# Kernel optimization log

Measured on AMD Instinct MI355X. Metric: run time of the kernel, lower is better.

## Reference

```python
import jax, jax.numpy as jnp
import numpy as np

N = 100000      # number of edge features (rows of feats)
M = 800000      # number of triplets
HID = 128
HEADS = 8
DH = HID // HEADS


def setup_inputs() -> dict:
    key = jax.random.key(0)
    ks = jax.random.split(key, 10)
    s = 1.0 / np.sqrt(HID)
    inp = {
        "feats": jax.random.normal(ks[0], (N, HID), dtype=jnp.float32),
        "idx_kj": jax.random.randint(ks[1], (M,), 0, N, dtype=jnp.int64),
        "idx_ji": jax.random.randint(ks[2], (M,), 0, N, dtype=jnp.int64),
        "Wv": jax.random.uniform(ks[3], (HID, HID), jnp.float32, -s, s),
        "Wq": jax.random.uniform(ks[4], (HID, HID), jnp.float32, -s, s),
        "Wk": jax.random.uniform(ks[5], (HID, HID), jnp.float32, -s, s),
        "W1": jax.random.uniform(ks[6], (HID, HID), jnp.float32, -s, s),
        "b1": jax.random.uniform(ks[7], (HID,), jnp.float32, -s, s),
        "W2": jax.random.uniform(ks[8], (HID, HID), jnp.float32, -s, s),
        "b2": jax.random.uniform(ks[9], (HID,), jnp.float32, -s, s),
    }
    return inp


def reference(feats, idx_kj, idx_ji, Wv, Wq, Wk, W1, b1, W2, b2):
    # Projections (no bias), reshape to [N, H, Dh]
    v = (feats @ Wv.T).reshape(N, HEADS, DH)
    k = (feats @ Wk.T).reshape(N, HEADS, DH)
    q = (feats @ Wq.T).reshape(N, HEADS, DH)

    # edge-indexed attention scores: [M, H, 1]
    att = jnp.sum(q[idx_kj] * k[idx_ji], axis=-1, keepdims=True)
    att = jnp.exp(jax.nn.leaky_relu(att, negative_slope=0.2))  # unsafe softmax, as in source

    # segment-sum normalizer over destination index idx_ji: [N, H, 1]
    denom = jax.ops.segment_sum(att, idx_ji, num_segments=N)
    att = att / denom[idx_ji]

    # weighted V gather-scatter: [M, HID] -> [N, HID]
    v_att = (v[idx_kj] * att).reshape(M, HID)
    agg = jax.ops.segment_sum(v_att, idx_ji, num_segments=N)  # v_clone after +scatter-v

    v_flat = v.reshape(N, HID)
    # ResidualLayer (dropout in eval mode -> identity): v + relu(lin2(relu(lin1(agg))))
    h = jax.nn.relu(agg @ W1.T + b1)
    h = jax.nn.relu(h @ W2.T + b2)
    return v_flat + h
```

## Files before the change

### kernel.cpp

```cpp
#include <hip/hip_runtime.h>
#include <hip/hip_bf16.h>
#include <math.h>

#define N_NODES 100000
#define M_EDGES 800000
#define HID 128
#define HEADS 8
#define DH 16
#define SCAN_NB ((N_NODES + 1023) / 1024)

typedef __attribute__((ext_vector_type(8))) short short8;
typedef __attribute__((ext_vector_type(4))) float floatx4;

__device__ __forceinline__ ushort f32_to_bf16(float x) {
    __hip_bfloat16 h = __float2bfloat16(x);
    union { __hip_bfloat16 h; ushort u; } c; c.h = h;
    return c.u;
}
__device__ __forceinline__ float bf16_bits_to_f32(ushort u) {
    union { unsigned int i; float f; } c; c.i = ((unsigned int)u) << 16;
    return c.f;
}
__device__ __forceinline__ float bf16pair_lo(unsigned int p) {
    union { unsigned int i; float f; } c; c.i = p << 16; return c.f;
}
__device__ __forceinline__ float bf16pair_hi(unsigned int p) {
    union { unsigned int i; float f; } c; c.i = p & 0xffff0000u; return c.f;
}

__device__ __forceinline__ void stage_w_frag(const ushort* __restrict__ W,
                                             ushort* __restrict__ lds, int tid)
{
    #pragma unroll
    for (int i = 0; i < 8; ++i) {
        int idx  = i * 256 + tid;
        int f    = idx >> 6;
        int lane = idx & 63;
        int t    = f & 7, ks = f >> 3;
        int row  = t * 16 + (lane & 15);
        int col  = ks * 32 + (lane >> 4) * 8;
        uint4 d = *(const uint4*)(W + row * HID + col);
        *(uint4*)(lds + idx * 8) = d;
    }
}

__global__ __launch_bounds__(256) void cvt_w_kernel(
    const float* __restrict__ Wq, const float* __restrict__ Wk, const float* __restrict__ Wv,
    const float* __restrict__ W1, const float* __restrict__ W2,
    ushort* __restrict__ dq, ushort* __restrict__ dk, ushort* __restrict__ dv,
    ushort* __restrict__ d1, ushort* __restrict__ d2)
{
    int i = blockIdx.x * 256 + threadIdx.x;
    int w = i >> 14;
    int j = i & 16383;
    const float* s[5] = {Wq, Wk, Wv, W1, W2};
    ushort*      d[5] = {dq, dk, dv, d1, d2};
    d[w][j] = f32_to_bf16(s[w][j]);
}

__global__ __launch_bounds__(256) void qkv_mfma_kernel(
    const float* __restrict__ feats,
    const ushort* __restrict__ Wq16, const ushort* __restrict__ Wk16, const ushort* __restrict__ Wv16,
    ushort* __restrict__ qv16, ushort* __restrict__ k16)
{
    __shared__ ushort wlds[16384];
    const int tid  = threadIdx.x;
    const int wave = tid >> 6;
    const int lane = tid & 63;
    const int row0 = blockIdx.x * 128 + wave * 32;
    const int lrow = lane & 15;
    const int lk   = (lane >> 4) * 8;
    const int crow = (lane >> 4) * 4;

    short8 afrag[2][4];
    bool tvalid[2];
    #pragma unroll
    for (int r = 0; r < 2; ++r) {
        int rr = row0 + r * 16;
        tvalid[r] = (rr < N_NODES);
        const float* arow = feats + (size_t)((tvalid[r] ? rr : 0) + lrow) * HID + lk;
        #pragma unroll
        for (int ks = 0; ks < 4; ++ks) {
            float4 f0 = *(const float4*)(arow + ks * 32);
            float4 f1 = *(const float4*)(arow + ks * 32 + 4);
            short8 a;
            a[0] = (short)f32_to_bf16(f0.x); a[1] = (short)f32_to_bf16(f0.y);
            a[2] = (short)f32_to_bf16(f0.z); a[3] = (short)f32_to_bf16(f0.w);
            a[4] = (short)f32_to_bf16(f1.x); a[5] = (short)f32_to_bf16(f1.y);
            a[6] = (short)f32_to_bf16(f1.z); a[7] = (short)f32_to_bf16(f1.w);
            afrag[r][ks] = a;
        }
    }

    const ushort* Ws[3] = {Wq16, Wk16, Wv16};
    ushort* Ob[3]; int Ostride[3];
    Ob[0] = qv16;       Ostride[0] = 256;
    Ob[1] = k16;        Ostride[1] = 128;
    Ob[2] = qv16 + 128; Ostride[2] = 256;

    #pragma unroll
    for (int w = 0; w < 3; ++w) {
        __syncthreads();
        stage_w_frag(Ws[w], wlds, tid);
        __syncthreads();

        floatx4 acc[2][8];
        #pragma unroll
        for (int r = 0; r < 2; ++r)
            #pragma unroll
            for (int t = 0; t < 8; ++t) acc[r][t] = (floatx4)(0.f);

        #pragma unroll
        for (int ks = 0; ks < 4; ++ks) {
            short8 B[8];
            #pragma unroll
            for (int t = 0; t < 8; ++t)
                B[t] = *(const short8*)&wlds[(ks * 8 + t) * 512 + lane * 8];
            #pragma unroll
            for (int t = 0; t < 8; ++t) {
                acc[0][t] = __builtin_amdgcn_mfma_f32_16x16x32_bf16(B[t], afrag[0][ks], acc[0][t], 0, 0, 0);
                acc[1][t] = __builtin_amdgcn_mfma_f32_16x16x32_bf16(B[t], afrag[1][ks], acc[1][t], 0, 0, 0);
            }
        }

        #pragma unroll
        for (int r = 0; r < 2; ++r) {
            if (tvalid[r]) {
                ushort* O = Ob[w] + (size_t)(row0 + r * 16 + lrow) * Ostride[w];
                #pragma unroll
                for (int t = 0; t < 8; ++t) {
                    ushort4 o;
                    o.x = f32_to_bf16(acc[r][t][0]); o.y = f32_to_bf16(acc[r][t][1]);
                    o.z = f32_to_bf16(acc[r][t][2]); o.w = f32_to_bf16(acc[r][t][3]);
                    *(ushort4*)(O + t * 16 + crow) = o;
                }
            }
        }
    }
}

__global__ __launch_bounds__(256) void hist_kernel(
    const int* __restrict__ idx_ji, int* __restrict__ count)
{
    int m = blockIdx.x * 256 + threadIdx.x;
    if (m < M_EDGES) atomicAdd(&count[idx_ji[m]], 1);
}

__global__ __launch_bounds__(256) void scan_blocksum_kernel(
    const int* __restrict__ count, int* __restrict__ blocksum)
{
    __shared__ int s[256];
    const int tid = threadIdx.x;
    const int base = blockIdx.x * 1024 + tid * 4;
    int sum = 0;
    if (base + 3 < N_NODES) {
        int4 c = *(const int4*)(count + base);
        sum = c.x + c.y + c.z + c.w;
    } else {
        #pragma unroll
        for (int j = 0; j < 4; ++j) if (base + j < N_NODES) sum += count[base + j];
    }
    s[tid] = sum;
    __syncthreads();
    for (int off = 128; off > 0; off >>= 1) {
        if (tid < off) s[tid] += s[tid + off];
        __syncthreads();
    }
    if (tid == 0) blocksum[blockIdx.x] = s[0];
}

__global__ __launch_bounds__(128) void scan_top_kernel(int* __restrict__ blocksum)
{
    __shared__ int s[128];
    const int t = threadIdx.x;
    int v = (t < SCAN_NB) ? blocksum[t] : 0;
    s[t] = v;
    __syncthreads();
    for (int off = 1; off < 128; off <<= 1) {
        int x = (t >= off) ? s[t - off] : 0;
        __syncthreads();
        s[t] += x;
        __syncthreads();
    }
    if (t < SCAN_NB) blocksum[t] = s[t] - v;
}

__global__ __launch_bounds__(256) void scan_write_kernel(
    const int* __restrict__ count, const int* __restrict__ blocksum,
    int* __restrict__ offsets, int* __restrict__ cursor)
{
    __shared__ int s[256];
    const int tid = threadIdx.x;
    const int base = blockIdx.x * 1024 + tid * 4;
    int c0 = 0, c1 = 0, c2 = 0, c3 = 0;
    if (base + 3 < N_NODES) {
        int4 c = *(const int4*)(count + base);
        c0 = c.x; c1 = c.y; c2 = c.z; c3 = c.w;
    } else {
        if (base     < N_NODES) c0 = count[base];
        if (base + 1 < N_NODES) c1 = count[base + 1];
        if (base + 2 < N_NODES) c2 = count[base + 2];
        if (base + 3 < N_NODES) c3 = count[base + 3];
    }
    const int tsum = c0 + c1 + c2 + c3;
    s[tid] = tsum;
    __syncthreads();
    for (int off = 1; off < 256; off <<= 1) {
        int x = (tid >= off) ? s[tid - off] : 0;
        __syncthreads();
        s[tid] += x;
        __syncthreads();
    }
    int o0 = s[tid] - tsum + blocksum[blockIdx.x];
    int o1 = o0 + c0, o2 = o1 + c1, o3 = o2 + c2;
    if (base + 3 < N_NODES) {
        *(int4*)(offsets + base) = make_int4(o0, o1, o2, o3);
        *(int4*)(cursor  + base) = make_int4(o0, o1, o2, o3);
    } else {
        if (base     < N_NODES) { offsets[base]     = o0; cursor[base]     = o0; }
        if (base + 1 < N_NODES) { offsets[base + 1] = o1; cursor[base + 1] = o1; }
        if (base + 2 < N_NODES) { offsets[base + 2] = o2; cursor[base + 2] = o2; }
        if (base + 3 < N_NODES) { offsets[base + 3] = o3; cursor[base + 3] = o3; }
    }
}

__global__ __launch_bounds__(256) void fill_kernel(
    const int* __restrict__ idx_ji, const int* __restrict__ idx_kj,
    int* __restrict__ cursor, int* __restrict__ edge_kj)
{
    int m = blockIdx.x * 256 + threadIdx.x;
    if (m < M_EDGES) {
        int pos = atomicAdd(&cursor[idx_ji[m]], 1);
        edge_kj[pos] = idx_kj[m];
    }
}

__global__ __launch_bounds__(256) void aggregate_kernel(
    const int* __restrict__ edge_kj, const int* __restrict__ offsets,
    const int* __restrict__ count, const ushort* __restrict__ qv16,
    const ushort* __restrict__ k16, ushort* __restrict__ agg16)
{
    const int gid  = blockIdx.x * 256 + threadIdx.x;
    const int node = gid >> 4;
    const int l16  = threadIdx.x & 15;
    if (node >= N_NODES) return;

    const int deg  = count[node];
    const int base = offsets[node];

    float kn[8];
    {
        uint4 kp = *(const uint4*)(k16 + (size_t)node * HID + l16 * 8);
        const unsigned int* kw = (const unsigned int*)&kp;
        #pragma unroll
        for (int j = 0; j < 4; ++j) {
            kn[2*j]   = bf16pair_lo(kw[j]);
            kn[2*j+1] = bf16pair_hi(kw[j]);
        }
    }

    float acc[8] = {0.f,0.f,0.f,0.f,0.f,0.f,0.f,0.f};
    float d = 0.f;

    int e = 0;
    for (; e + 2 <= deg; e += 2) {
        const int kj0 = edge_kj[base + e];
        const int kj1 = edge_kj[base + e + 1];
        const ushort* r0 = qv16 + (size_t)kj0 * 256 + l16 * 8;
        const ushort* r1 = qv16 + (size_t)kj1 * 256 + l16 * 8;
        uint4 qp0 = *(const uint4*)r0;
        uint4 vp0 = *(const uint4*)(r0 + 128);
        uint4 qp1 = *(const uint4*)r1;
        uint4 vp1 = *(const uint4*)(r1 + 128);

        const unsigned int* q0 = (const unsigned int*)&qp0;
        const unsigned int* q1 = (const unsigned int*)&qp1;
        float p0 = 0.f, p1 = 0.f;
        #pragma unroll
        for (int j = 0; j < 4; ++j) {
            p0 += bf16pair_lo(q0[j]) * kn[2*j] + bf16pair_hi(q0[j]) * kn[2*j+1];
            p1 += bf16pair_lo(q1[j]) * kn[2*j] + bf16pair_hi(q1[j]) * kn[2*j+1];
        }
        p0 += __shfl_xor(p0, 1);
        p1 += __shfl_xor(p1, 1);
        float lr0 = (p0 >= 0.f) ? p0 : 0.2f * p0;
        float lr1 = (p1 >= 0.f) ? p1 : 0.2f * p1;
        float s0 = __expf(lr0);
        float s1 = __expf(lr1);
        d += s0 + s1;
        const unsigned int* v0 = (const unsigned int*)&vp0;
        const unsigned int* v1 = (const unsigned int*)&vp1;
        #pragma unroll
        for (int j = 0; j < 4; ++j) {
            acc[2*j]   += s0 * bf16pair_lo(v0[j]) + s1 * bf16pair_lo(v1[j]);
            acc[2*j+1] += s0 * bf16pair_hi(v0[j]) + s1 * bf16pair_hi(v1[j]);
        }
    }
    if (e < deg) {
        const int kj0 = edge_kj[base + e];
        const ushort* r0 = qv16 + (size_t)kj0 * 256 + l16 * 8;
        uint4 qp0 = *(const uint4*)r0;
        uint4 vp0 = *(const uint4*)(r0 + 128);
        const unsigned int* q0 = (const unsigned int*)&qp0;
        float p0 = 0.f;
        #pragma unroll
        for (int j = 0; j < 4; ++j)
            p0 += bf16pair_lo(q0[j]) * kn[2*j] + bf16pair_hi(q0[j]) * kn[2*j+1];
        p0 += __shfl_xor(p0, 1);
        float lr0 = (p0 >= 0.f) ? p0 : 0.2f * p0;
        float s0 = __expf(lr0);
        d += s0;
        const unsigned int* v0 = (const unsigned int*)&vp0;
        #pragma unroll
        for (int j = 0; j < 4; ++j) {
            acc[2*j]   += s0 * bf16pair_lo(v0[j]);
            acc[2*j+1] += s0 * bf16pair_hi(v0[j]);
        }
    }

    const float inv = (deg > 0) ? 1.f / d : 0.f;
    uint4 o;
    unsigned int* ow = (unsigned int*)&o;
    #pragma unroll
    for (int j = 0; j < 4; ++j)
        ow[j] = (unsigned int)f32_to_bf16(acc[2*j] * inv)
              | ((unsigned int)f32_to_bf16(acc[2*j+1] * inv) << 16);
    *(uint4*)(agg16 + (size_t)node * HID + l16 * 8) = o;
}

__global__ __launch_bounds__(256) void mlp_mfma_kernel(
    const ushort* __restrict__ agg16, const ushort* __restrict__ qv16,
    const ushort* __restrict__ W1_16, const float* __restrict__ b1,
    const ushort* __restrict__ W2_16, const float* __restrict__ b2,
    float* __restrict__ out)
{
    __shared__ ushort wlds[16384];
    __shared__ ushort h1s[16384];
    const int tid  = threadIdx.x;
    const int wave = tid >> 6;
    const int lane = tid & 63;
    const int row0 = blockIdx.x * 128 + wave * 32;
    const int lrow = lane & 15;
    const int lk   = (lane >> 4) * 8;
    const int crow = (lane >> 4) * 4;

    short8 afrag[2][4];
    bool tvalid[2];
    #pragma unroll
    for (int r = 0; r < 2; ++r) {
        int rr = row0 + r * 16;
        tvalid[r] = (rr < N_NODES);
        const ushort* arow = agg16 + (size_t)((tvalid[r] ? rr : 0) + lrow) * HID + lk;
        #pragma unroll
        for (int ks = 0; ks < 4; ++ks)
            afrag[r][ks] = *(const short8*)(arow + ks * 32);
    }

    stage_w_frag(W1_16, wlds, tid);
    __syncthreads();

    {
        floatx4 acc[2][8];
        #pragma unroll
        for (int r = 0; r < 2; ++r)
            #pragma unroll
            for (int t = 0; t < 8; ++t) acc[r][t] = (floatx4)(0.f);
        #pragma unroll
        for (int ks = 0; ks < 4; ++ks) {
            short8 B[8];
            #pragma unroll
            for (int t = 0; t < 8; ++t)
                B[t] = *(const short8*)&wlds[(ks * 8 + t) * 512 + lane * 8];
            #pragma unroll
            for (int t = 0; t < 8; ++t) {
                acc[0][t] = __builtin_amdgcn_mfma_f32_16x16x32_bf16(B[t], afrag[0][ks], acc[0][t], 0, 0, 0);
                acc[1][t] = __builtin_amdgcn_mfma_f32_16x16x32_bf16(B[t], afrag[1][ks], acc[1][t], 0, 0, 0);
            }
        }
        #pragma unroll
        for (int r = 0; r < 2; ++r) {
            ushort* tile = &h1s[(wave * 2 + r) * 2048];
            #pragma unroll
            for (int t = 0; t < 8; ++t) {
                float4 bias = *(const float4*)(b1 + t * 16 + crow);
                ushort4 o;
                o.x = f32_to_bf16(fmaxf(acc[r][t][0] + bias.x, 0.f));
                o.y = f32_to_bf16(fmaxf(acc[r][t][1] + bias.y, 0.f));
                o.z = f32_to_bf16(fmaxf(acc[r][t][2] + bias.z, 0.f));
                o.w = f32_to_bf16(fmaxf(acc[r][t][3] + bias.w, 0.f));
                int ks   = t >> 1;
                int quad = (t & 1) * 2 + (crow >> 3);
                int j0   = crow & 4;
                *(ushort4*)(tile + (ks * 64 + quad * 16 + lrow) * 8 + j0) = o;
            }
        }
    }
    __syncthreads();
    stage_w_frag(W2_16, wlds, tid);
    __syncthreads();

    {
        short8 hfrag[2][4];
        #pragma unroll
        for (int r = 0; r < 2; ++r) {
            const ushort* tile = &h1s[(wave * 2 + r) * 2048];
            #pragma unroll
            for (int ks = 0; ks < 4; ++ks)
                hfrag[r][ks] = *(const short8*)(tile + (ks * 64 + lane) * 8);
        }
        floatx4 acc[2][8];
        #pragma unroll
        for (int r = 0; r < 2; ++r)
            #pragma unroll
            for (int t = 0; t < 8; ++t) acc[r][t] = (floatx4)(0.f);
        #pragma unroll
        for (int ks = 0; ks < 4; ++ks) {
            short8 B[8];
            #pragma unroll
            for (int t = 0; t < 8; ++t)
                B[t] = *(const short8*)&wlds[(ks * 8 + t) * 512 + lane * 8];
            #pragma unroll
            for (int t = 0; t < 8; ++t) {
                acc[0][t] = __builtin_amdgcn_mfma_f32_16x16x32_bf16(B[t], hfrag[0][ks], acc[0][t], 0, 0, 0);
                acc[1][t] = __builtin_amdgcn_mfma_f32_16x16x32_bf16(B[t], hfrag[1][ks], acc[1][t], 0, 0, 0);
            }
        }
        #pragma unroll
        for (int r = 0; r < 2; ++r) {
            if (tvalid[r]) {
                const size_t nrow = (size_t)(row0 + r * 16 + lrow);
                const ushort* vrow = qv16 + nrow * 256 + 128;
                float* orow = out + nrow * HID;
                #pragma unroll
                for (int t = 0; t < 8; ++t) {
                    float4 bias = *(const float4*)(b2 + t * 16 + crow);
                    ushort4 vv = *(const ushort4*)(vrow + t * 16 + crow);
                    float4 o;
                    o.x = bf16_bits_to_f32(vv.x) + fmaxf(acc[r][t][0] + bias.x, 0.f);
                    o.y = bf16_bits_to_f32(vv.y) + fmaxf(acc[r][t][1] + bias.y, 0.f);
                    o.z = bf16_bits_to_f32(vv.z) + fmaxf(acc[r][t][2] + bias.z, 0.f);
                    o.w = bf16_bits_to_f32(vv.w) + fmaxf(acc[r][t][3] + bias.w, 0.f);
                    *(float4*)(orow + t * 16 + crow) = o;
                }
            }
        }
    }
}

extern "C" void kernel_launch(void* const* d_in, const int* in_sizes, int n_in,
                              void* d_out, int out_size, void* d_ws, size_t ws_size,
                              hipStream_t stream) {
    const float* feats  = (const float*)d_in[0];
    const int*   idx_kj = (const int*)d_in[1];
    const int*   idx_ji = (const int*)d_in[2];
    const float* Wv     = (const float*)d_in[3];
    const float* Wq     = (const float*)d_in[4];
    const float* Wk     = (const float*)d_in[5];
    const float* W1     = (const float*)d_in[6];
    const float* b1     = (const float*)d_in[7];
    const float* W2     = (const float*)d_in[8];
    const float* b2     = (const float*)d_in[9];
    float* out = (float*)d_out;

    ushort* qv16    = (ushort*)d_ws;
    ushort* k16     = qv16    + (size_t)N_NODES * 256;
    ushort* agg16   = k16     + (size_t)N_NODES * HID;
    ushort* Wq16    = agg16   + (size_t)N_NODES * HID;
    ushort* Wk16    = Wq16 + HID * HID;
    ushort* Wv16    = Wk16 + HID * HID;
    ushort* W116    = Wv16 + HID * HID;
    ushort* W216    = W116 + HID * HID;
    int* count      = (int*)(W216 + HID * HID);
    int* offsets    = count + N_NODES;
    int* cursor     = offsets + N_NODES;
    int* blocksum   = cursor + N_NODES;
    int* edge_kj    = blocksum + ((SCAN_NB + 3) & ~3);

    hipMemsetAsync(count, 0, N_NODES * sizeof(int), stream);

    cvt_w_kernel<<<(5 * HID * HID + 255) / 256, 256, 0, stream>>>(
        Wq, Wk, Wv, W1, W2, Wq16, Wk16, Wv16, W116, W216);

    qkv_mfma_kernel<<<(N_NODES + 127) / 128, 256, 0, stream>>>(
        feats, Wq16, Wk16, Wv16, qv16, k16);

    hist_kernel<<<(M_EDGES + 255) / 256, 256, 0, stream>>>(idx_ji, count);
    scan_blocksum_kernel<<<SCAN_NB, 256, 0, stream>>>(count, blocksum);
    scan_top_kernel<<<1, 128, 0, stream>>>(blocksum);
    scan_write_kernel<<<SCAN_NB, 256, 0, stream>>>(count, blocksum, offsets, cursor);
    fill_kernel<<<(M_EDGES + 255) / 256, 256, 0, stream>>>(idx_ji, idx_kj, cursor, edge_kj);

    aggregate_kernel<<<((size_t)N_NODES * 16 + 255) / 256, 256, 0, stream>>>(
        edge_kj, offsets, count, qv16, k16, agg16);

    mlp_mfma_kernel<<<(N_NODES + 127) / 128, 256, 0, stream>>>(
        agg16, qv16, W116, b1, W216, b2, out);
}
```

Baseline: 327.5 us.

## Sort nodes by degree for balanced aggregation and unroll edge loop by four

Adds a counting sort of destination nodes by in-degree (histogram, scan, scatter into a permutation that reuses the cursor buffer), so each wavefront's 16-lane groups handle nodes with similar edge counts and less time is lost to divergent loop trip counts. The aggregation loop is also unrolled to four edges per iteration to keep more independent gathers in flight. The cost is three extra small kernel launches, an indirection through perm, and a scattered write order for agg16 that loses locality in node order.

```diff
diff --git a/kernel.cpp b/kernel.cpp
--- a/kernel.cpp
+++ b/kernel.cpp
@@ -8,6 +8,7 @@
 #define HEADS 8
 #define DH 16
 #define SCAN_NB ((N_NODES + 1023) / 1024)
+#define DBINS 64
 
 typedef __attribute__((ext_vector_type(8))) short short8;
 typedef __attribute__((ext_vector_type(4))) float floatx4;
@@ -235,15 +236,85 @@
     }
 }
 
+__global__ __launch_bounds__(256) void deg_hist_kernel(
+    const int* __restrict__ count, int* __restrict__ dhist)
+{
+    __shared__ int h[DBINS];
+    const int tid = threadIdx.x;
+    if (tid < DBINS) h[tid] = 0;
+    __syncthreads();
+    int n = blockIdx.x * 256 + tid;
+    if (n < N_NODES) atomicAdd(&h[min(count[n], DBINS - 1)], 1);
+    __syncthreads();
+    if (tid < DBINS && h[tid]) atomicAdd(&dhist[tid], h[tid]);
+}
+
+__global__ __launch_bounds__(64) void deg_scan_kernel(
+    const int* __restrict__ dhist, int* __restrict__ dcursor)
+{
+    __shared__ int s[DBINS];
+    const int t = threadIdx.x;
+    int v = dhist[t];
+    s[t] = v;
+    __syncthreads();
+    for (int off = 1; off < DBINS; off <<= 1) {
+        int x = (t >= off) ? s[t - off] : 0;
+        __syncthreads();
+        s[t] += x;
+        __syncthreads();
+    }
+    dcursor[t] = s[t] - v;
+}
+
+__global__ __launch_bounds__(256) void deg_scatter_kernel(
+    const int* __restrict__ count, int* __restrict__ dcursor,
+    int* __restrict__ perm)
+{
+    __shared__ int h[DBINS];
+    __shared__ int b[DBINS];
+    const int tid = threadIdx.x;
+    if (tid < DBINS) h[tid] = 0;
+    __syncthreads();
+    int n = blockIdx.x * 256 + tid;
+    int d = -1, r = 0;
+    if (n < N_NODES) {
+        d = min(count[n], DBINS - 1);
+        r = atomicAdd(&h[d], 1);
+    }
+    __syncthreads();
+    if (tid < DBINS && h[tid]) b[tid] = atomicAdd(&dcursor[tid], h[tid]);
+    __syncthreads();
+    if (n < N_NODES) perm[b[d] + r] = n;
+}
+
+__device__ __forceinline__ float dot8(const uint4& qp, const float* kn) {
+    const unsigned int* q = (const unsigned int*)&qp;
+    float p = 0.f;
+    #pragma unroll
+    for (int j = 0; j < 4; ++j)
+        p += bf16pair_lo(q[j]) * kn[2*j] + bf16pair_hi(q[j]) * kn[2*j+1];
+    return p;
+}
+__device__ __forceinline__ void axpy8(float* acc, float s, const uint4& vp) {
+    const unsigned int* v = (const unsigned int*)&vp;
+    #pragma unroll
+    for (int j = 0; j < 4; ++j) {
+        acc[2*j]   += s * bf16pair_lo(v[j]);
+        acc[2*j+1] += s * bf16pair_hi(v[j]);
+    }
+}
+
 __global__ __launch_bounds__(256) void aggregate_kernel(
     const int* __restrict__ edge_kj, const int* __restrict__ offsets,
-    const int* __restrict__ count, const ushort* __restrict__ qv16,
+    const int* __restrict__ count, const int* __restrict__ perm,
+    const ushort* __restrict__ qv16,
     const ushort* __restrict__ k16, ushort* __restrict__ agg16)
 {
     const int gid  = blockIdx.x * 256 + threadIdx.x;
-    const int node = gid >> 4;
+    const int slot = gid >> 4;
     const int l16  = threadIdx.x & 15;
-    if (node >= N_NODES) return;
+    if (slot >= N_NODES) return;
+    const int node = perm[slot];
 
     const int deg  = count[node];
     const int base = offsets[node];
@@ -262,60 +333,68 @@
     float acc[8] = {0.f,0.f,0.f,0.f,0.f,0.f,0.f,0.f};
     float d = 0.f;
 
+    const ushort* qvb = qv16 + l16 * 8;
+
     int e = 0;
-    for (; e + 2 <= deg; e += 2) {
+    for (; e + 4 <= deg; e += 4) {
+        const int kj0 = edge_kj[base + e + 0];
+        const int kj1 = edge_kj[base + e + 1];
+        const int kj2 = edge_kj[base + e + 2];
+        const int kj3 = edge_kj[base + e + 3];
+        const ushort* r0 = qvb + (size_t)kj0 * 256;
+        const ushort* r1 = qvb + (size_t)kj1 * 256;
+        const ushort* r2 = qvb + (size_t)kj2 * 256;
+        const ushort* r3 = qvb + (size_t)kj3 * 256;
+        uint4 qp0 = *(const uint4*)r0;  uint4 vp0 = *(const uint4*)(r0 + 128);
+        uint4 qp1 = *(const uint4*)r1;  uint4 vp1 = *(const uint4*)(r1 + 128);
+        uint4 qp2 = *(const uint4*)r2;  uint4 vp2 = *(const uint4*)(r2 + 128);
+        uint4 qp3 = *(const uint4*)r3;  uint4 vp3 = *(const uint4*)(r3 + 128);
+
+        float p0 = dot8(qp0, kn);
+        float p1 = dot8(qp1, kn);
+        float p2 = dot8(qp2, kn);
+        float p3 = dot8(qp3, kn);
+        p0 += __shfl_xor(p0, 1);
+        p1 += __shfl_xor(p1, 1);
+        p2 += __shfl_xor(p2, 1);
+        p3 += __shfl_xor(p3, 1);
+        float s0 = __expf(fmaxf(p0, 0.2f * p0));
+        float s1 = __expf(fmaxf(p1, 0.2f * p1));
+        float s2 = __expf(fmaxf(p2, 0.2f * p2));
+        float s3 = __expf(fmaxf(p3, 0.2f * p3));
+        d += (s0 + s1) + (s2 + s3);
+        axpy8(acc, s0, vp0);
+        axpy8(acc, s1, vp1);
+        axpy8(acc, s2, vp2);
+        axpy8(acc, s3, vp3);
+    }
+    if (e + 2 <= deg) {
         const int kj0 = edge_kj[base + e];
         const int kj1 = edge_kj[base + e + 1];
-        const ushort* r0 = qv16 + (size_t)kj0 * 256 + l16 * 8;
-        const ushort* r1 = qv16 + (size_t)kj1 * 256 + l16 * 8;
-        uint4 qp0 = *(const uint4*)r0;
-        uint4 vp0 = *(const uint4*)(r0 + 128);
-        uint4 qp1 = *(const uint4*)r1;
-        uint4 vp1 = *(const uint4*)(r1 + 128);
-
-        const unsigned int* q0 = (const unsigned int*)&qp0;
-        const unsigned int* q1 = (const unsigned int*)&qp1;
-        float p0 = 0.f, p1 = 0.f;
-        #pragma unroll
-        for (int j = 0; j < 4; ++j) {
-            p0 += bf16pair_lo(q0[j]) * kn[2*j] + bf16pair_hi(q0[j]) * kn[2*j+1];
-            p1 += bf16pair_lo(q1[j]) * kn[2*j] + bf16pair_hi(q1[j]) * kn[2*j+1];
-        }
+        const ushort* r0 = qvb + (size_t)kj0 * 256;
+        const ushort* r1 = qvb + (size_t)kj1 * 256;
+        uint4 qp0 = *(const uint4*)r0;  uint4 vp0 = *(const uint4*)(r0 + 128);
+        uint4 qp1 = *(const uint4*)r1;  uint4 vp1 = *(const uint4*)(r1 + 128);
+        float p0 = dot8(qp0, kn);
+        float p1 = dot8(qp1, kn);
         p0 += __shfl_xor(p0, 1);
         p1 += __shfl_xor(p1, 1);
-        float lr0 = (p0 >= 0.f) ? p0 : 0.2f * p0;
-        float lr1 = (p1 >= 0.f) ? p1 : 0.2f * p1;
-        float s0 = __expf(lr0);
-        float s1 = __expf(lr1);
+        float s0 = __expf(fmaxf(p0, 0.2f * p0));
+        float s1 = __expf(fmaxf(p1, 0.2f * p1));
         d += s0 + s1;
-        const unsigned int* v0 = (const unsigned int*)&vp0;
-        const unsigned int* v1 = (const unsigned int*)&vp1;
-        #pragma unroll
-        for (int j = 0; j < 4; ++j) {
-            acc[2*j]   += s0 * bf16pair_lo(v0[j]) + s1 * bf16pair_lo(v1[j]);
-            acc[2*j+1] += s0 * bf16pair_hi(v0[j]) + s1 * bf16pair_hi(v1[j]);
-        }
+        axpy8(acc, s0, vp0);
+        axpy8(acc, s1, vp1);
+        e += 2;
     }
     if (e < deg) {
         const int kj0 = edge_kj[base + e];
-        const ushort* r0 = qv16 + (size_t)kj0 * 256 + l16 * 8;
-        uint4 qp0 = *(const uint4*)r0;
-        uint4 vp0 = *(const uint4*)(r0 + 128);
-        const unsigned int* q0 = (const unsigned int*)&qp0;
-        float p0 = 0.f;
-        #pragma unroll
-        for (int j = 0; j < 4; ++j)
-            p0 += bf16pair_lo(q0[j]) * kn[2*j] + bf16pair_hi(q0[j]) * kn[2*j+1];
+        const ushort* r0 = qvb + (size_t)kj0 * 256;
+        uint4 qp0 = *(const uint4*)r0;  uint4 vp0 = *(const uint4*)(r0 + 128);
+        float p0 = dot8(qp0, kn);
         p0 += __shfl_xor(p0, 1);
-        float lr0 = (p0 >= 0.f) ? p0 : 0.2f * p0;
-        float s0 = __expf(lr0);
+        float s0 = __expf(fmaxf(p0, 0.2f * p0));
         d += s0;
-        const unsigned int* v0 = (const unsigned int*)&vp0;
-        #pragma unroll
-        for (int j = 0; j < 4; ++j) {
-            acc[2*j]   += s0 * bf16pair_lo(v0[j]);
-            acc[2*j+1] += s0 * bf16pair_hi(v0[j]);
-        }
+        axpy8(acc, s0, vp0);
     }
 
     const float inv = (deg > 0) ? 1.f / d : 0.f;
@@ -475,8 +554,12 @@
     int* cursor     = offsets + N_NODES;
     int* blocksum   = cursor + N_NODES;
     int* edge_kj    = blocksum + ((SCAN_NB + 3) & ~3);
+    int* dhist      = edge_kj + M_EDGES;
+    int* dcursor    = dhist + DBINS;
+    int* perm       = cursor;
 
     hipMemsetAsync(count, 0, N_NODES * sizeof(int), stream);
+    hipMemsetAsync(dhist, 0, DBINS * sizeof(int), stream);
 
     cvt_w_kernel<<<(5 * HID * HID + 255) / 256, 256, 0, stream>>>(
         Wq, Wk, Wv, W1, W2, Wq16, Wk16, Wv16, W116, W216);
@@ -490,8 +573,12 @@
     scan_write_kernel<<<SCAN_NB, 256, 0, stream>>>(count, blocksum, offsets, cursor);
     fill_kernel<<<(M_EDGES + 255) / 256, 256, 0, stream>>>(idx_ji, idx_kj, cursor, edge_kj);
 
+    deg_hist_kernel<<<(N_NODES + 255) / 256, 256, 0, stream>>>(count, dhist);
+    deg_scan_kernel<<<1, DBINS, 0, stream>>>(dhist, dcursor);
+    deg_scatter_kernel<<<(N_NODES + 255) / 256, 256, 0, stream>>>(count, dcursor, perm);
+
     aggregate_kernel<<<((size_t)N_NODES * 16 + 255) / 256, 256, 0, stream>>>(
-        edge_kj, offsets, count, qv16, k16, agg16);
+        edge_kj, offsets, count, perm, qv16, k16, agg16);
 
     mlp_mfma_kernel<<<(N_NODES + 127) / 128, 256, 0, stream>>>(
         agg16, qv16, W116, b1, W216, b2, out);
```

New measurement: 349.8 us. 6.8% more time.
